# Kernel optimization log

Measured on AMD Instinct MI355X. Metric: run time of the kernel, lower is better.

Reference implementation:

```python
import jax, jax.numpy as jnp
import numpy as np

H, M, D, O, N = 16, 1024, 512, 512, 16384


def setup_inputs() -> dict:
    key = jax.random.key(0)
    ks = jax.random.split(key, 8)
    inp = {
        "k": jax.random.normal(ks[0], (N, O), dtype=jnp.float32),
        "mems": jax.random.normal(ks[1], (H, M, D), dtype=jnp.float32),
        "Wk": jax.random.normal(ks[2], (H, O, D), dtype=jnp.float32) * (1.0 / np.sqrt(D)),
        "bk": jax.random.normal(ks[3], (H, O), dtype=jnp.float32) * 0.02,
        "Wv": jax.random.normal(ks[4], (H, O, D), dtype=jnp.float32) * (1.0 / np.sqrt(D)),
        "bv": jax.random.normal(ks[5], (H, O), dtype=jnp.float32) * 0.02,
        "Wf": jax.random.normal(ks[6], (O, H * O), dtype=jnp.float32) * (1.0 / np.sqrt(H * O)),
        "bf": jax.random.normal(ks[7], (O,), dtype=jnp.float32) * 0.02,
    }
    return inp


def reference(k, mems, Wk, bk, Wv, bv, Wf, bf):
    # Batched over heads. Per head h:
    #   key_h = softmax(mem_h @ Wk_h^T + bk_h)  -> [M, O]
    #   val_h = mem_h @ Wv_h^T + bv_h           -> [M, O]
    #   att_h = softmax(k @ key_h^T)            -> [N, M]
    #   out_h = att_h @ val_h                   -> [N, O]
    key_logits = jnp.einsum("hmd,hod->hmo", mems, Wk) + bk[:, None, :]
    mem_key = jax.nn.softmax(key_logits, axis=-1)            # [H, M, O]
    mem_val = jnp.einsum("hmd,hod->hmo", mems, Wv) + bv[:, None, :]  # [H, M, O]
    att = jnp.einsum("no,hmo->hnm", k, mem_key)              # [H, N, M]
    att_w = jax.nn.softmax(att, axis=-1)
    out_h = jnp.einsum("hnm,hmo->hno", att_w, mem_val)       # [H, N, O]
    # torch.cat(outputs, dim=-1): head h occupies columns [h*O:(h+1)*O]
    x = jnp.transpose(out_h, (1, 0, 2)).reshape(N, H * O)    # [N, H*O]
    return x @ Wf.T + bf                                     # [N, O]
```

## Files before the change

kernel.cpp:

```cpp
#include <hip/hip_runtime.h>
#include <math.h>

typedef unsigned short u16;
typedef __attribute__((ext_vector_type(8))) short short8;
typedef __attribute__((ext_vector_type(4))) float floatx4;

#define Hh 16
#define Mm 1024
#define Dd 512
#define Oo 512
#define Nn 16384

__device__ __forceinline__ float b2f(u16 u) { return __uint_as_float(((unsigned)u) << 16); }
__device__ __forceinline__ u16 f2b(float f) {
    unsigned v = __float_as_uint(f);
    v += 0x7fffu + ((v >> 16) & 1u);
    return (u16)(v >> 16);
}
__device__ __forceinline__ short8 cvt8(const float* p) {
    float4 a = *(const float4*)p, b = *(const float4*)(p + 4);
    u16 o[8];
    o[0] = f2b(a.x); o[1] = f2b(a.y); o[2] = f2b(a.z); o[3] = f2b(a.w);
    o[4] = f2b(b.x); o[5] = f2b(b.y); o[6] = f2b(b.z); o[7] = f2b(b.w);
    return *(short8*)o;
}

__global__ __launch_bounds__(256) void gemm_bt(
    const void* __restrict__ A, const void* __restrict__ B, const float* __restrict__ bias,
    void* __restrict__ C, int K, int lda, int ldb, int ldc,
    long sA, long sB, long sBias, long sC, int aF32, int bF32, int outBf)
{
    __shared__ u16 At[64][72];
    __shared__ u16 Bt[64][72];
    const int tid = threadIdx.x, lane = tid & 63, wid = tid >> 6;
    const int m0 = blockIdx.y * 64, n0 = blockIdx.x * 64;
    const int h = blockIdx.z;
    const int wm = wid >> 1, wn = wid & 1;
    const int rl = lane & 15, rq = (lane >> 4) * 4, gl8 = (lane >> 4) * 8;

    floatx4 zero4 = {0.f, 0.f, 0.f, 0.f};
    floatx4 acc[2][2];
    acc[0][0] = zero4; acc[0][1] = zero4; acc[1][0] = zero4; acc[1][1] = zero4;

    for (int k0 = 0; k0 < K; k0 += 64) {
#pragma unroll
        for (int i = 0; i < 2; i++) {
            int c = tid + i * 256;
            int r = c >> 3, cc = (c & 7) * 8;
            long aoff = (long)h * sA + (long)(m0 + r) * lda + k0 + cc;
            long boff = (long)h * sB + (long)(n0 + r) * ldb + k0 + cc;
            *(short8*)&At[r][cc] = aF32 ? cvt8((const float*)A + aoff)
                                        : *(const short8*)((const u16*)A + aoff);
            *(short8*)&Bt[r][cc] = bF32 ? cvt8((const float*)B + boff)
                                        : *(const short8*)((const u16*)B + boff);
        }
        __syncthreads();
#pragma unroll
        for (int ks = 0; ks < 2; ks++) {
            short8 a0 = *(const short8*)&At[wm * 32 + rl][ks * 32 + gl8];
            short8 a1 = *(const short8*)&At[wm * 32 + 16 + rl][ks * 32 + gl8];
            short8 b0 = *(const short8*)&Bt[wn * 32 + rl][ks * 32 + gl8];
            short8 b1 = *(const short8*)&Bt[wn * 32 + 16 + rl][ks * 32 + gl8];
            acc[0][0] = __builtin_amdgcn_mfma_f32_16x16x32_bf16(a0, b0, acc[0][0], 0, 0, 0);
            acc[0][1] = __builtin_amdgcn_mfma_f32_16x16x32_bf16(a0, b1, acc[0][1], 0, 0, 0);
            acc[1][0] = __builtin_amdgcn_mfma_f32_16x16x32_bf16(a1, b0, acc[1][0], 0, 0, 0);
            acc[1][1] = __builtin_amdgcn_mfma_f32_16x16x32_bf16(a1, b1, acc[1][1], 0, 0, 0);
        }
        __syncthreads();
    }

#pragma unroll
    for (int i = 0; i < 2; i++)
#pragma unroll
        for (int j = 0; j < 2; j++) {
            int col = n0 + wn * 32 + j * 16 + rl;
            float bb = bias ? bias[(long)h * sBias + col] : 0.f;
#pragma unroll
            for (int r = 0; r < 4; r++) {
                int row = m0 + wm * 32 + i * 16 + rq + r;
                long idx = (long)h * sC + (long)row * ldc + col;
                float v = acc[i][j][r] + bb;
                if (outBf) ((u16*)C)[idx] = f2b(v);
                else       ((float*)C)[idx] = v;
            }
        }
}

__global__ __launch_bounds__(256) void softmax_rows(const float* __restrict__ L, u16* __restrict__ Kout)
{
    const int tid = threadIdx.x, lane = tid & 63, wid = tid >> 6;
    const long row = (long)blockIdx.x * 4 + wid;
    const float* p = L + row * 512 + lane * 8;
    float v[8];
    *(float4*)&v[0] = *(const float4*)p;
    *(float4*)&v[4] = *(const float4*)(p + 4);
    float mx = v[0];
#pragma unroll
    for (int i = 1; i < 8; i++) mx = fmaxf(mx, v[i]);
    for (int d = 1; d < 64; d <<= 1) mx = fmaxf(mx, __shfl_xor(mx, d));
    float s = 0.f;
#pragma unroll
    for (int i = 0; i < 8; i++) { v[i] = __expf(v[i] - mx); s += v[i]; }
    for (int d = 1; d < 64; d <<= 1) s += __shfl_xor(s, d);
    float inv = 1.f / s;
    u16 o[8];
#pragma unroll
    for (int i = 0; i < 8; i++) o[i] = f2b(v[i] * inv);
    *(short8*)(Kout + row * 512 + lane * 8) = *(short8*)o;
}

#define LDQ 520
#define LDP 520
#define FLASH_LDS ((64 * LDQ + 64 * LDP) * 2 + 2 * 64 * 4 + 16)

__global__ __launch_bounds__(512, 2) void flash(
    const float* __restrict__ kq, const u16* __restrict__ key,
    const u16* __restrict__ vpt, const float* __restrict__ bfv, float* __restrict__ out)
{
    extern __shared__ u16 sm[];
    u16* kq_s = sm;
    u16* Ph = sm + 64 * LDQ;
    float* lbuf = (float*)(sm + 64 * (LDQ + LDP));

    const int tid = threadIdx.x, lane = tid & 63, wid = tid >> 6;
    const int n0 = blockIdx.x * 64;
    const int rl = lane & 15, rq = (lane >> 4) * 4, gl8 = (lane >> 4) * 8;

#pragma unroll
    for (int i = 0; i < 8; i++) {
        int c = tid + i * 512;
        int r = c >> 6, cc = (c & 63) * 8;
        *(short8*)&kq_s[r * LDQ + cc] = cvt8(&kq[(long)(n0 + r) * 512 + cc]);
    }
    if (tid < 128) lbuf[tid] = 0.f;
    __syncthreads();

    floatx4 zero4 = {0.f, 0.f, 0.f, 0.f};
    floatx4 oacc[4][4], utmp[4][4];
#pragma unroll
    for (int i = 0; i < 4; i++)
#pragma unroll
        for (int j = 0; j < 4; j++) { oacc[i][j] = zero4; utmp[i][j] = zero4; }

    for (int h = 0; h < Hh; h++) {
        const u16* keyh = key + (long)h * Mm * Oo;
        const u16* vph = vpt + (long)h * Oo * Mm;
        float* lcur = lbuf + (h & 1) * 64;
        float* lnxt = lbuf + ((h + 1) & 1) * 64;

        for (int hf = 0; hf < 2; hf++) {
            float psum[4][4];
#pragma unroll
            for (int qt = 0; qt < 4; qt++)
#pragma unroll
                for (int r = 0; r < 4; r++) psum[qt][r] = 0.f;

            for (int t = 0; t < 4; t++) {
                int mb = hf * 512 + wid * 64 + t * 16;
                const u16* bp = keyh + (long)(mb + rl) * 512 + gl8;
                floatx4 s[4];
#pragma unroll
                for (int qt = 0; qt < 4; qt++) s[qt] = zero4;
#pragma unroll
                for (int ks = 0; ks < 16; ks++) {
                    short8 b = *(const short8*)(bp + ks * 32);
#pragma unroll
                    for (int qt = 0; qt < 4; qt++) {
                        short8 a = *(const short8*)&kq_s[(qt * 16 + rl) * LDQ + ks * 32 + gl8];
                        s[qt] = __builtin_amdgcn_mfma_f32_16x16x32_bf16(a, b, s[qt], 0, 0, 0);
                    }
                }
                int colP = wid * 64 + t * 16 + rl;
#pragma unroll
                for (int qt = 0; qt < 4; qt++)
#pragma unroll
                    for (int r = 0; r < 4; r++) {
                        float e = __expf(s[qt][r]);
                        psum[qt][r] += e;
                        Ph[(qt * 16 + rq + r) * LDP + colP] = f2b(e);
                    }
            }
            for (int d = 1; d < 16; d <<= 1)
#pragma unroll
                for (int qt = 0; qt < 4; qt++)
#pragma unroll
                    for (int r = 0; r < 4; r++) psum[qt][r] += __shfl_xor(psum[qt][r], d);
            if (rl == 0)
#pragma unroll
                for (int qt = 0; qt < 4; qt++)
#pragma unroll
                    for (int r = 0; r < 4; r++)
                        atomicAdd(&lcur[qt * 16 + rq + r], psum[qt][r]);
            if (hf == 0 && tid < 64) lnxt[tid] = 0.f;
            __syncthreads();

            const u16* vbp[4];
#pragma unroll
            for (int ot = 0; ot < 4; ot++)
                vbp[ot] = vph + (long)(wid * 64 + ot * 16 + rl) * Mm + hf * 512 + gl8;
#pragma unroll 4
            for (int mk = 0; mk < 16; mk++) {
                short8 a[4], b[4];
#pragma unroll
                for (int qt = 0; qt < 4; qt++)
                    a[qt] = *(const short8*)&Ph[(qt * 16 + rl) * LDP + mk * 32 + gl8];
#pragma unroll
                for (int ot = 0; ot < 4; ot++)
                    b[ot] = *(const short8*)(vbp[ot] + mk * 32);
#pragma unroll
                for (int qt = 0; qt < 4; qt++)
#pragma unroll
                    for (int ot = 0; ot < 4; ot++)
                        utmp[qt][ot] = __builtin_amdgcn_mfma_f32_16x16x32_bf16(a[qt], b[ot], utmp[qt][ot], 0, 0, 0);
            }

            if (hf == 1) {
#pragma unroll
                for (int qt = 0; qt < 4; qt++)
#pragma unroll
                    for (int r = 0; r < 4; r++) {
                        float inv = 1.f / lcur[qt * 16 + rq + r];
#pragma unroll
                        for (int ot = 0; ot < 4; ot++) {
                            oacc[qt][ot][r] += inv * utmp[qt][ot][r];
                            utmp[qt][ot][r] = 0.f;
                        }
                    }
            }
            __syncthreads();
        }
    }

#pragma unroll
    for (int qt = 0; qt < 4; qt++)
#pragma unroll
        for (int ot = 0; ot < 4; ot++) {
            int col = wid * 64 + ot * 16 + rl;
            float add = bfv[col];
#pragma unroll
            for (int r = 0; r < 4; r++) {
                int row = n0 + qt * 16 + rq + r;
                out[(long)row * 512 + col] = oacc[qt][ot][r] + add;
            }
        }
}

extern "C" void kernel_launch(void* const* d_in, const int* in_sizes, int n_in,
                              void* d_out, int out_size, void* d_ws, size_t ws_size,
                              hipStream_t stream)
{
    const float* k    = (const float*)d_in[0];
    const void*  mems = d_in[1];
    const void*  Wk   = d_in[2];
    const float* bk   = (const float*)d_in[3];
    const void*  Wv   = d_in[4];
    const float* bv   = (const float*)d_in[5];
    const void*  Wf   = d_in[6];
    const float* bfv  = (const float*)d_in[7];
    float* out = (float*)d_out;

    char* ws = (char*)d_ws;
    float* logits = (float*)ws;
    u16* keyb = (u16*)(ws + (size_t)Hh * Mm * Oo * 4);
    u16* valb = keyb + (size_t)Hh * Mm * Oo;
    u16* vptb = valb + (size_t)Hh * Mm * Oo;

    gemm_bt<<<dim3(8, 16, 16), 256, 0, stream>>>(
        mems, Wk, bk, logits, 512, 512, 512, 512,
        (long)Mm * Dd, (long)Oo * Dd, 512L, (long)Mm * Oo, 1, 1, 0);

    softmax_rows<<<dim3(Hh * Mm / 4), 256, 0, stream>>>(logits, keyb);

    gemm_bt<<<dim3(8, 16, 16), 256, 0, stream>>>(
        mems, Wv, bv, valb, 512, 512, 512, 512,
        (long)Mm * Dd, (long)Oo * Dd, 512L, (long)Mm * Oo, 1, 1, 1);

    gemm_bt<<<dim3(16, 8, 16), 256, 0, stream>>>(
        Wf, valb, nullptr, vptb, 512, Hh * Oo, 512, 1024,
        512L, (long)Mm * Oo, 0L, (long)Oo * Mm, 1, 0, 1);

    flash<<<dim3(Nn / 64), 512, FLASH_LDS, stream>>>(k, keyb, vptb, bfv, out);
}
```

Before: 1.463 ms.

## Halve flash query tile to 32 rows, raise occupancy, replace LDS atomics

Shrinks each flash block from 64 to 32 query rows, which halves LDS and accumulator register use so launch bounds can ask for 4 blocks per CU. The softmax denominator is now built from per-wave partial sums reduced by 32 threads instead of LDS atomicAdd, and the MFMA loops are wrapped in s_setprio. The trade-off is that each key and value tile fetched from global/L2 now serves only half as many queries, doubling that traffic.

```diff
diff --git a/kernel.cpp b/kernel.cpp
--- a/kernel.cpp
+++ b/kernel.cpp
@@ -109,70 +109,71 @@
     *(short8*)(Kout + row * 512 + lane * 8) = *(short8*)o;
 }
 
+#define QB 32
 #define LDQ 520
 #define LDP 520
-#define FLASH_LDS ((64 * LDQ + 64 * LDP) * 2 + 2 * 64 * 4 + 16)
-
-__global__ __launch_bounds__(512, 2) void flash(
+#define FLASH_LDS (QB * LDQ * 2 + QB * LDP * 2 + 8 * 32 * 4 + 32 * 4)
+
+__global__ __launch_bounds__(512, 4) void flash(
     const float* __restrict__ kq, const u16* __restrict__ key,
     const u16* __restrict__ vpt, const float* __restrict__ bfv, float* __restrict__ out)
 {
     extern __shared__ u16 sm[];
     u16* kq_s = sm;
-    u16* Ph = sm + 64 * LDQ;
-    float* lbuf = (float*)(sm + 64 * (LDQ + LDP));
+    u16* Ph   = sm + QB * LDQ;
+    float* lpart = (float*)(sm + QB * (LDQ + LDP));
+    float* lfin  = lpart + 8 * 32;
 
     const int tid = threadIdx.x, lane = tid & 63, wid = tid >> 6;
-    const int n0 = blockIdx.x * 64;
+    const int n0 = blockIdx.x * QB;
     const int rl = lane & 15, rq = (lane >> 4) * 4, gl8 = (lane >> 4) * 8;
 
 #pragma unroll
-    for (int i = 0; i < 8; i++) {
+    for (int i = 0; i < 4; i++) {
         int c = tid + i * 512;
         int r = c >> 6, cc = (c & 63) * 8;
         *(short8*)&kq_s[r * LDQ + cc] = cvt8(&kq[(long)(n0 + r) * 512 + cc]);
     }
-    if (tid < 128) lbuf[tid] = 0.f;
     __syncthreads();
 
     floatx4 zero4 = {0.f, 0.f, 0.f, 0.f};
-    floatx4 oacc[4][4], utmp[4][4];
-#pragma unroll
-    for (int i = 0; i < 4; i++)
+    floatx4 oacc[2][4], utmp[2][4];
+#pragma unroll
+    for (int i = 0; i < 2; i++)
 #pragma unroll
         for (int j = 0; j < 4; j++) { oacc[i][j] = zero4; utmp[i][j] = zero4; }
 
     for (int h = 0; h < Hh; h++) {
         const u16* keyh = key + (long)h * Mm * Oo;
         const u16* vph = vpt + (long)h * Oo * Mm;
-        float* lcur = lbuf + (h & 1) * 64;
-        float* lnxt = lbuf + ((h + 1) & 1) * 64;
 
         for (int hf = 0; hf < 2; hf++) {
-            float psum[4][4];
-#pragma unroll
-            for (int qt = 0; qt < 4; qt++)
+            float psum[2][4];
+#pragma unroll
+            for (int qt = 0; qt < 2; qt++)
 #pragma unroll
                 for (int r = 0; r < 4; r++) psum[qt][r] = 0.f;
 
+#pragma unroll
             for (int t = 0; t < 4; t++) {
                 int mb = hf * 512 + wid * 64 + t * 16;
                 const u16* bp = keyh + (long)(mb + rl) * 512 + gl8;
-                floatx4 s[4];
-#pragma unroll
-                for (int qt = 0; qt < 4; qt++) s[qt] = zero4;
+                floatx4 s[2];
+                s[0] = zero4; s[1] = zero4;
+                __builtin_amdgcn_s_setprio(1);
 #pragma unroll
                 for (int ks = 0; ks < 16; ks++) {
                     short8 b = *(const short8*)(bp + ks * 32);
 #pragma unroll
-                    for (int qt = 0; qt < 4; qt++) {
+                    for (int qt = 0; qt < 2; qt++) {
                         short8 a = *(const short8*)&kq_s[(qt * 16 + rl) * LDQ + ks * 32 + gl8];
                         s[qt] = __builtin_amdgcn_mfma_f32_16x16x32_bf16(a, b, s[qt], 0, 0, 0);
                     }
                 }
+                __builtin_amdgcn_s_setprio(0);
                 int colP = wid * 64 + t * 16 + rl;
 #pragma unroll
-                for (int qt = 0; qt < 4; qt++)
+                for (int qt = 0; qt < 2; qt++)
 #pragma unroll
                     for (int r = 0; r < 4; r++) {
                         float e = __expf(s[qt][r]);
@@ -182,44 +183,57 @@
             }
             for (int d = 1; d < 16; d <<= 1)
 #pragma unroll
-                for (int qt = 0; qt < 4; qt++)
+                for (int qt = 0; qt < 2; qt++)
 #pragma unroll
                     for (int r = 0; r < 4; r++) psum[qt][r] += __shfl_xor(psum[qt][r], d);
-            if (rl == 0)
-#pragma unroll
-                for (int qt = 0; qt < 4; qt++)
-#pragma unroll
-                    for (int r = 0; r < 4; r++)
-                        atomicAdd(&lcur[qt * 16 + rq + r], psum[qt][r]);
-            if (hf == 0 && tid < 64) lnxt[tid] = 0.f;
+            if (rl == 0) {
+#pragma unroll
+                for (int qt = 0; qt < 2; qt++)
+#pragma unroll
+                    for (int r = 0; r < 4; r++) {
+                        int row = qt * 16 + rq + r;
+                        if (hf == 0) lpart[wid * 32 + row] = psum[qt][r];
+                        else         lpart[wid * 32 + row] += psum[qt][r];
+                    }
+            }
             __syncthreads();
+
+            if (hf == 1 && tid < 32) {
+                float sum = 0.f;
+#pragma unroll
+                for (int w = 0; w < 8; w++) sum += lpart[w * 32 + tid];
+                lfin[tid] = sum;
+            }
 
             const u16* vbp[4];
 #pragma unroll
             for (int ot = 0; ot < 4; ot++)
                 vbp[ot] = vph + (long)(wid * 64 + ot * 16 + rl) * Mm + hf * 512 + gl8;
+            __builtin_amdgcn_s_setprio(1);
 #pragma unroll 4
             for (int mk = 0; mk < 16; mk++) {
-                short8 a[4], b[4];
-#pragma unroll
-                for (int qt = 0; qt < 4; qt++)
+                short8 a[2], b[4];
+#pragma unroll
+                for (int qt = 0; qt < 2; qt++)
                     a[qt] = *(const short8*)&Ph[(qt * 16 + rl) * LDP + mk * 32 + gl8];
 #pragma unroll
                 for (int ot = 0; ot < 4; ot++)
                     b[ot] = *(const short8*)(vbp[ot] + mk * 32);
 #pragma unroll
-                for (int qt = 0; qt < 4; qt++)
+                for (int qt = 0; qt < 2; qt++)
 #pragma unroll
                     for (int ot = 0; ot < 4; ot++)
                         utmp[qt][ot] = __builtin_amdgcn_mfma_f32_16x16x32_bf16(a[qt], b[ot], utmp[qt][ot], 0, 0, 0);
             }
+            __builtin_amdgcn_s_setprio(0);
+            __syncthreads();
 
             if (hf == 1) {
 #pragma unroll
-                for (int qt = 0; qt < 4; qt++)
+                for (int qt = 0; qt < 2; qt++)
 #pragma unroll
                     for (int r = 0; r < 4; r++) {
-                        float inv = 1.f / lcur[qt * 16 + rq + r];
+                        float inv = 1.f / lfin[qt * 16 + rq + r];
 #pragma unroll
                         for (int ot = 0; ot < 4; ot++) {
                             oacc[qt][ot][r] += inv * utmp[qt][ot][r];
@@ -227,12 +241,11 @@
                         }
                     }
             }
-            __syncthreads();
         }
     }
 
 #pragma unroll
-    for (int qt = 0; qt < 4; qt++)
+    for (int qt = 0; qt < 2; qt++)
 #pragma unroll
         for (int ot = 0; ot < 4; ot++) {
             int col = wid * 64 + ot * 16 + rl;
@@ -279,5 +292,5 @@
         Wf, valb, nullptr, vptb, 512, Hh * Oo, 512, 1024,
         512L, (long)Mm * Oo, 0L, (long)Oo * Mm, 1, 0, 1);
 
-    flash<<<dim3(Nn / 64), 512, FLASH_LDS, stream>>>(k, keyb, vptb, bfv, out);
-}
+    flash<<<dim3(Nn / QB), 512, FLASH_LDS, stream>>>(k, keyb, vptb, bfv, out);
+}
```

Measured after the change: 2.075 ms. +41.8%, slower.

## Lockstep heads across blocks with grid sync and drop LDS atomics

Applied to the files above, without the earlier changes.

The flash kernel now runs as a cooperative launch and calls a grid-wide barrier after each head. This keeps all blocks working on the same head's key and value matrices at once, which is meant to improve L2 and MALL reuse. The per-row softmax denominators no longer use LDS atomicAdd into double buffers; each wave writes its partial sums to a per-wave slot and one reduction pass sums them. In exchange this adds fifteen grid-wide barriers and an extra block barrier per half-head, and it requires every block to be resident at the same time.

```diff
diff --git a/kernel.cpp b/kernel.cpp
--- a/kernel.cpp
+++ b/kernel.cpp
@@ -1,5 +1,8 @@
 #include <hip/hip_runtime.h>
+#include <hip/hip_cooperative_groups.h>
 #include <math.h>
+
+namespace cg = cooperative_groups;
 
 typedef unsigned short u16;
 typedef __attribute__((ext_vector_type(8))) short short8;
@@ -111,16 +114,18 @@
 
 #define LDQ 520
 #define LDP 520
-#define FLASH_LDS ((64 * LDQ + 64 * LDP) * 2 + 2 * 64 * 4 + 16)
+#define FLASH_LDS ((64 * LDQ + 64 * LDP) * 2 + 8 * 64 * 4 + 64 * 4)
 
 __global__ __launch_bounds__(512, 2) void flash(
     const float* __restrict__ kq, const u16* __restrict__ key,
     const u16* __restrict__ vpt, const float* __restrict__ bfv, float* __restrict__ out)
 {
+    cg::grid_group grid = cg::this_grid();
     extern __shared__ u16 sm[];
     u16* kq_s = sm;
-    u16* Ph = sm + 64 * LDQ;
-    float* lbuf = (float*)(sm + 64 * (LDQ + LDP));
+    u16* Ph   = sm + 64 * LDQ;
+    float* lpart = (float*)(sm + 64 * (LDQ + LDP));
+    float* lfin  = lpart + 8 * 64;
 
     const int tid = threadIdx.x, lane = tid & 63, wid = tid >> 6;
     const int n0 = blockIdx.x * 64;
@@ -132,7 +137,6 @@
         int r = c >> 6, cc = (c & 63) * 8;
         *(short8*)&kq_s[r * LDQ + cc] = cvt8(&kq[(long)(n0 + r) * 512 + cc]);
     }
-    if (tid < 128) lbuf[tid] = 0.f;
     __syncthreads();
 
     floatx4 zero4 = {0.f, 0.f, 0.f, 0.f};
@@ -145,8 +149,6 @@
     for (int h = 0; h < Hh; h++) {
         const u16* keyh = key + (long)h * Mm * Oo;
         const u16* vph = vpt + (long)h * Oo * Mm;
-        float* lcur = lbuf + (h & 1) * 64;
-        float* lnxt = lbuf + ((h + 1) & 1) * 64;
 
         for (int hf = 0; hf < 2; hf++) {
             float psum[4][4];
@@ -185,14 +187,24 @@
                 for (int qt = 0; qt < 4; qt++)
 #pragma unroll
                     for (int r = 0; r < 4; r++) psum[qt][r] += __shfl_xor(psum[qt][r], d);
-            if (rl == 0)
-#pragma unroll
-                for (int qt = 0; qt < 4; qt++)
-#pragma unroll
-                    for (int r = 0; r < 4; r++)
-                        atomicAdd(&lcur[qt * 16 + rq + r], psum[qt][r]);
-            if (hf == 0 && tid < 64) lnxt[tid] = 0.f;
+            if (rl == 0) {
+#pragma unroll
+                for (int qt = 0; qt < 4; qt++)
+#pragma unroll
+                    for (int r = 0; r < 4; r++) {
+                        int row = qt * 16 + rq + r;
+                        if (hf == 0) lpart[wid * 64 + row] = psum[qt][r];
+                        else         lpart[wid * 64 + row] += psum[qt][r];
+                    }
+            }
             __syncthreads();
+
+            if (hf == 1 && tid < 64) {
+                float sum = 0.f;
+#pragma unroll
+                for (int w = 0; w < 8; w++) sum += lpart[w * 64 + tid];
+                lfin[tid] = sum;
+            }
 
             const u16* vbp[4];
 #pragma unroll
@@ -213,13 +225,14 @@
                     for (int ot = 0; ot < 4; ot++)
                         utmp[qt][ot] = __builtin_amdgcn_mfma_f32_16x16x32_bf16(a[qt], b[ot], utmp[qt][ot], 0, 0, 0);
             }
+            __syncthreads();
 
             if (hf == 1) {
 #pragma unroll
                 for (int qt = 0; qt < 4; qt++)
 #pragma unroll
                     for (int r = 0; r < 4; r++) {
-                        float inv = 1.f / lcur[qt * 16 + rq + r];
+                        float inv = 1.f / lfin[qt * 16 + rq + r];
 #pragma unroll
                         for (int ot = 0; ot < 4; ot++) {
                             oacc[qt][ot][r] += inv * utmp[qt][ot][r];
@@ -227,8 +240,9 @@
                         }
                     }
             }
-            __syncthreads();
-        }
+        }
+
+        if (h < Hh - 1) grid.sync();
     }
 
 #pragma unroll
@@ -279,5 +293,7 @@
         Wf, valb, nullptr, vptb, 512, Hh * Oo, 512, 1024,
         512L, (long)Mm * Oo, 0L, (long)Oo * Mm, 1, 0, 1);
 
-    flash<<<dim3(Nn / 64), 512, FLASH_LDS, stream>>>(k, keyb, vptb, bfv, out);
-}
+    void* kargs[] = { (void*)&k, (void*)&keyb, (void*)&vptb, (void*)&bfv, (void*)&out };
+    hipLaunchCooperativeKernel((void*)flash, dim3(Nn / 64), dim3(512),
+                               kargs, (unsigned)FLASH_LDS, stream);
+}
```

Result: slower. 1.791 ms (+22.4%).
